# Performance work log

Hardware: AMD Instinct MI355X
Metric: run time of the kernel (lower is better)

The kernel has to match this reference:

```python
import jax, jax.numpy as jnp
import numpy as np

D_IN = 256
D_OUT = 256

def setup_inputs() -> dict:
    key = jax.random.key(0)
    kx, kq, kk, kv = jax.random.split(key, 4)
    x = jax.random.normal(kx, (8, D_IN, 64, 64), dtype=jnp.float32)
    s = 1.0 / np.sqrt(D_IN)
    Wq = jax.random.normal(kq, (D_OUT, D_IN), dtype=jnp.float32) * s
    Wk = jax.random.normal(kk, (D_OUT, D_IN), dtype=jnp.float32) * s
    Wv = jax.random.normal(kv, (D_OUT, D_IN), dtype=jnp.float32) * s
    return {"x": x, "Wq": Wq, "Wk": Wk, "Wv": Wv}

def reference(x, Wq, Wk, Wv):
    b, c_in, h, w = x.shape
    c = Wq.shape[0]
    # 1x1 conv == channel linear; tokens along N = h*w
    xt = x.reshape(b, c_in, h * w).transpose(0, 2, 1)      # (b, N, c_in)
    q = jnp.einsum('bnc,dc->bnd', xt, Wq)                  # (b, N, c)
    k = jnp.einsum('bnc,dc->bnd', xt, Wk)
    v = jnp.einsum('bnc,dc->bnd', xt, Wv)
    wei = jnp.einsum('bnd,bmd->bnm', q, k) / jnp.sqrt(jnp.asarray(c, x.dtype))
    wei = jax.nn.softmax(wei, axis=-1)
    out = jnp.einsum('bnm,bmd->bnd', wei, v)               # (b, N, c)
    return out.transpose(0, 2, 1).reshape(b, c, h, w)
```

## Files before the change

### kernel.cpp

```cpp
#include <hip/hip_runtime.h>

#define DIN 256
#define NTOK 4096

typedef __bf16 bf16;
typedef __bf16 bf16x4 __attribute__((ext_vector_type(4)));
typedef __bf16 bf16x8 __attribute__((ext_vector_type(8)));
typedef float floatx16 __attribute__((ext_vector_type(16)));

__device__ inline floatx16 mfma32(bf16x8 a, bf16x8 b, floatx16 c) {
    return __builtin_amdgcn_mfma_f32_32x32x16_bf16(a, b, c, 0, 0, 0);
}

__device__ inline void async16(const void* g, void* l) {
    __builtin_amdgcn_global_load_lds(
        (const __attribute__((address_space(1))) unsigned int*)g,
        (__attribute__((address_space(3))) unsigned int*)l, 16, 0, 0);
}

__global__ void convert_w(const float* __restrict__ wq, const float* __restrict__ wk,
                          const float* __restrict__ wv, bf16* __restrict__ Wb) {
    int i = blockIdx.x * 256 + threadIdx.x;
    const float* src = (i < 65536) ? wq : (i < 131072 ? wk : wv);
    Wb[i] = (bf16)src[i & 65535];
}

__global__ __launch_bounds__(512, 2) void proj_kernel(
    const float* __restrict__ x, const bf16* __restrict__ Wb,
    bf16* __restrict__ Qo, bf16* __restrict__ Ko, bf16* __restrict__ Vo)
{
    __shared__ __attribute__((aligned(16))) char smem[131072];
    bf16 (*xs)[264] = (bf16(*)[264])smem;
    bf16* bufA = (bf16*)smem;
    bf16* bufB = (bf16*)(smem + 65536);

    int bid = blockIdx.x;
    int b = bid & 7, nt = bid >> 3;
    int n0 = nt * 128;
    int t = threadIdx.x;
    int lane = t & 63, w = t >> 6;
    int l32 = lane & 31, h = lane >> 5;
    int tokg = w >> 1;
    int og   = w & 1;

    int wofs[8];
#pragma unroll
    for (int jj = 0; jj < 8; ++jj) {
        int q = w * 8 + jj;
        int r2 = 2 * q + h;
        int cs = l32 ^ (r2 & 31);
        wofs[jj] = r2 * 512 + cs * 16;
    }

    {
        const float* xb = x + (size_t)b * DIN * NTOK;
#pragma unroll
        for (int it = 0; it < 16; ++it) {
            int flat = it * 512 + t;
            int c = flat >> 5;
            int nf = flat & 31;
            float4 v = *(const float4*)(xb + (size_t)c * NTOK + n0 + nf * 4);
            int nn = nf * 4;
            xs[nn + 0][c] = (bf16)v.x;
            xs[nn + 1][c] = (bf16)v.y;
            xs[nn + 2][c] = (bf16)v.z;
            xs[nn + 3][c] = (bf16)v.w;
        }
    }
    __syncthreads();

    bf16x8 xf[16];
#pragma unroll
    for (int ks = 0; ks < 16; ++ks)
        xf[ks] = *(const bf16x8*)&xs[tokg * 32 + l32][ks * 16 + h * 8];

    __syncthreads();

    {
        const char* src = (const char*)Wb;
#pragma unroll
        for (int jj = 0; jj < 8; ++jj)
            async16(src + wofs[jj], (char*)bufA + (w * 8 + jj) * 1024);
    }
    __syncthreads();

    for (int p = 0; p < 6; ++p) {
        if (p < 5) {
            bf16* nb = ((p + 1) & 1) ? bufB : bufA;
            const char* src = (const char*)Wb + (size_t)(p + 1) * 65536;
#pragma unroll
            for (int jj = 0; jj < 8; ++jj)
                async16(src + wofs[jj], (char*)nb + (w * 8 + jj) * 1024);
        }

        const bf16* wb = (p & 1) ? bufB : bufA;
        int mat = p >> 1, dhalf = p & 1;

        floatx16 acc[2];
#pragma unroll
        for (int dc = 0; dc < 2; ++dc)
#pragma unroll
            for (int i = 0; i < 16; ++i) acc[dc][i] = 0.0f;

        if (mat < 2) {
#pragma unroll
            for (int ks = 0; ks < 16; ++ks) {
#pragma unroll
                for (int dc = 0; dc < 2; ++dc) {
                    int row = og * 64 + dc * 32 + l32;
                    bf16x8 wf = *(const bf16x8*)((const char*)wb + row * 512 +
                                                 (((2 * ks + h) ^ (row & 31)) * 16));
                    acc[dc] = mfma32(xf[ks], wf, acc[dc]);
                }
            }
            bf16* Out = (mat == 0 ? Qo : Ko) + (size_t)b * NTOK * DIN;
#pragma unroll
            for (int dc = 0; dc < 2; ++dc) {
                int d = dhalf * 128 + og * 64 + dc * 32 + l32;
#pragma unroll
                for (int r = 0; r < 16; ++r) {
                    int tok = n0 + tokg * 32 + (r & 3) + 8 * (r >> 2) + 4 * h;
                    Out[(size_t)tok * DIN + d] = (bf16)acc[dc][r];
                }
            }
        } else {
#pragma unroll
            for (int ks = 0; ks < 16; ++ks) {
#pragma unroll
                for (int dc = 0; dc < 2; ++dc) {
                    int row = og * 64 + dc * 32 + l32;
                    bf16x8 wf = *(const bf16x8*)((const char*)wb + row * 512 +
                                                 (((2 * ks + h) ^ (row & 31)) * 16));
                    acc[dc] = mfma32(wf, xf[ks], acc[dc]);
                }
            }
            bf16* Out = Vo + (size_t)b * DIN * NTOK;
            int tok = n0 + tokg * 32 + l32;
#pragma unroll
            for (int dc = 0; dc < 2; ++dc)
#pragma unroll
                for (int r = 0; r < 16; ++r) {
                    int d = dhalf * 128 + og * 64 + dc * 32 + (r & 3) + 8 * (r >> 2) + 4 * h;
                    Out[(size_t)d * NTOK + tok] = (bf16)acc[dc][r];
                }
        }
        __syncthreads();
    }
}

__global__ __launch_bounds__(768, 3) void attn_kernel(
    const bf16* __restrict__ Q, const bf16* __restrict__ K,
    const bf16* __restrict__ V, float* __restrict__ out)
{
    __shared__ bf16 Ks[2][64][256];
    __shared__ bf16 Vs[2][256][64];
    __shared__ bf16 Ps[2][128][64];

    int bid = blockIdx.x;
    int b = bid & 7, qt = bid >> 3;
    int n0 = qt * 128;
    int t = threadIdx.x, lane = t & 63, w = t >> 6;
    int l32 = lane & 31, h = lane >> 5;
    int lkey = (l32 & 7) ^ ((l32 >> 3) & 3);

    const bf16* Qb = Q + (size_t)b * NTOK * DIN;
    const bf16* Kb = K + (size_t)b * NTOK * DIN;
    const bf16* Vb = V + (size_t)b * DIN * NTOK;
    float* Lp = (float*)&Ps[0][0][0];

    if (w < 4) {
        int qg = w;

        int koff[8];
#pragma unroll
        for (int jj = 0; jj < 8; ++jj) {
            int q = w * 8 + jj;
            int r = q * 2 + h;
            int ck = l32 ^ ((r & 7) ^ ((r >> 3) & 3));
            koff[jj] = (r * 256 + ck * 8) * 2;
        }

        bf16x8 qf[16];
        {
            const bf16* qrow = Qb + (size_t)(n0 + qg * 32 + l32) * DIN + h * 8;
#pragma unroll
            for (int ks = 0; ks < 16; ++ks) qf[ks] = *(const bf16x8*)(qrow + ks * 16);
        }

        float lsum = 0.0f;

#pragma unroll
        for (int jj = 0; jj < 8; ++jj) {
            async16((const char*)Kb + koff[jj], (bf16*)Ks[0] + (w * 8 + jj) * 512);
            async16((const char*)Kb + 32768 + koff[jj], (bf16*)Ks[1] + (w * 8 + jj) * 512);
        }
        __syncthreads();

        {
            const bf16* Krd = (const bf16*)Ks[0] + l32 * 256;
            floatx16 st0, st1;
#pragma unroll
            for (int i = 0; i < 16; ++i) { st0[i] = 0.0f; st1[i] = 0.0f; }
#pragma unroll
            for (int ks = 0; ks < 16; ++ks) {
                int co = ((2 * ks + h) ^ lkey) * 8;
                bf16x8 kf0 = *(const bf16x8*)(Krd + co);
                bf16x8 kf1 = *(const bf16x8*)(Krd + 32 * 256 + co);
                st0 = mfma32(kf0, qf[ks], st0);
                st1 = mfma32(kf1, qf[ks], st1);
            }
            bf16* Prow = (bf16*)Ps[0] + (qg * 32 + l32) * 64;
#pragma unroll
            for (int kvb = 0; kvb < 2; ++kvb) {
#pragma unroll
                for (int g = 0; g < 4; ++g) {
                    bf16x4 pk;
#pragma unroll
                    for (int i = 0; i < 4; ++i) {
                        float sval = kvb ? st1[g * 4 + i] : st0[g * 4 + i];
                        float e = __expf(sval * 0.0625f);
                        lsum += e;
                        pk[i] = (bf16)e;
                    }
                    *(bf16x4*)((char*)Prow + (((kvb * 4 + g) ^ lkey) * 16) + h * 8) = pk;
                }
            }
        }
        __syncthreads();

#pragma unroll 1
        for (int mt = 0; mt < 64; ++mt) {
            if (mt < 62) {
                int kadd = (mt + 2) * 32768;
#pragma unroll
                for (int jj = 0; jj < 8; ++jj)
                    async16((const char*)Kb + kadd + koff[jj],
                            (bf16*)Ks[mt & 1] + (w * 8 + jj) * 512);
            }
            if (mt < 63) {
                const bf16* Krd = (const bf16*)Ks[(mt + 1) & 1] + l32 * 256;
                floatx16 st0, st1;
#pragma unroll
                for (int i = 0; i < 16; ++i) { st0[i] = 0.0f; st1[i] = 0.0f; }
#pragma unroll
                for (int ks = 0; ks < 16; ++ks) {
                    int co = ((2 * ks + h) ^ lkey) * 8;
                    bf16x8 kf0 = *(const bf16x8*)(Krd + co);
                    bf16x8 kf1 = *(const bf16x8*)(Krd + 32 * 256 + co);
                    st0 = mfma32(kf0, qf[ks], st0);
                    st1 = mfma32(kf1, qf[ks], st1);
                }
                bf16* Prow = (bf16*)Ps[(mt + 1) & 1] + (qg * 32 + l32) * 64;
#pragma unroll
                for (int kvb = 0; kvb < 2; ++kvb) {
#pragma unroll
                    for (int g = 0; g < 4; ++g) {
                        bf16x4 pk;
#pragma unroll
                        for (int i = 0; i < 4; ++i) {
                            float sval = kvb ? st1[g * 4 + i] : st0[g * 4 + i];
                            float e = __expf(sval * 0.0625f);
                            lsum += e;
                            pk[i] = (bf16)e;
                        }
                        *(bf16x4*)((char*)Prow + (((kvb * 4 + g) ^ lkey) * 16) + h * 8) = pk;
                    }
                }
            }
            __syncthreads();
        }

        {
            float sv = lsum;
            sv += __shfl_xor(sv, 32);
            if (h == 0) Lp[qg * 32 + l32] = sv;
        }
        __syncthreads();
    } else {
        int ws = w - 4;
        int slab2 = ws >> 1;
        int qh = ws & 1;

        int vofs[4];
#pragma unroll
        for (int jj = 0; jj < 4; ++jj) {
            int q = ws * 4 + jj;
            int d = q * 8 + (lane >> 3);
            int cv = (lane & 7) ^ ((d & 7) ^ ((d >> 3) & 3));
            vofs[jj] = (d * 4096 + cv * 8) * 2;
        }

        floatx16 oacc[4];
#pragma unroll
        for (int i = 0; i < 4; ++i)
            for (int j = 0; j < 16; ++j) oacc[i][j] = 0.0f;

#pragma unroll
        for (int jj = 0; jj < 4; ++jj)
            async16((const char*)Vb + vofs[jj], (bf16*)Vs[0] + (ws * 4 + jj) * 512);
        __syncthreads();
        __syncthreads();

#pragma unroll 1
        for (int mt = 0; mt < 64; ++mt) {
            if (mt < 63) {
                int vadd = (mt + 1) * 128;
#pragma unroll
                for (int jj = 0; jj < 4; ++jj)
                    async16((const char*)Vb + vadd + vofs[jj],
                            (bf16*)Vs[(mt + 1) & 1] + (ws * 4 + jj) * 512);
            }
            const bf16* Vrd = (const bf16*)Vs[mt & 1];
            const char* Prd = (const char*)Ps[mt & 1];
#pragma unroll
            for (int kst = 0; kst < 4; ++kst) {
                int co = ((kst * 2 + h) ^ lkey);
                int d0 = slab2 * 64 + l32;
                bf16x8 va0 = *(const bf16x8*)(Vrd + d0 * 64 + co * 8);
                bf16x8 va1 = *(const bf16x8*)(Vrd + (d0 + 32) * 64 + co * 8);
                bf16x8 pb0 = *(const bf16x8*)(Prd + (qh * 64 + l32) * 128 + co * 16);
                bf16x8 pb1 = *(const bf16x8*)(Prd + (qh * 64 + 32 + l32) * 128 + co * 16);
                oacc[0] = mfma32(va0, pb0, oacc[0]);
                oacc[1] = mfma32(va0, pb1, oacc[1]);
                oacc[2] = mfma32(va1, pb0, oacc[2]);
                oacc[3] = mfma32(va1, pb1, oacc[3]);
            }
            __syncthreads();
        }

        __syncthreads();
        float* ob = out + (size_t)b * DIN * NTOK;
#pragma unroll
        for (int tc = 0; tc < 2; ++tc) {
            int tokl = qh * 64 + tc * 32 + l32;
            float rinv = 1.0f / Lp[tokl];
#pragma unroll
            for (int dc = 0; dc < 2; ++dc)
#pragma unroll
                for (int r = 0; r < 16; ++r) {
                    int d = slab2 * 64 + dc * 32 + (r & 3) + 8 * (r >> 2) + 4 * h;
                    ob[(size_t)d * NTOK + n0 + tokl] = oacc[dc * 2 + tc][r] * rinv;
                }
        }
    }
}

extern "C" void kernel_launch(void* const* d_in, const int* in_sizes, int n_in,
                              void* d_out, int out_size, void* d_ws, size_t ws_size,
                              hipStream_t stream) {
    const float* x  = (const float*)d_in[0];
    const float* wq = (const float*)d_in[1];
    const float* wk = (const float*)d_in[2];
    const float* wv = (const float*)d_in[3];
    float* outf = (float*)d_out;

    char* ws = (char*)d_ws;
    bf16* Wb = (bf16*)(ws);
    bf16* Qp = (bf16*)(ws + (1u << 20));
    bf16* Kp = (bf16*)(ws + (1u << 20) + (16u << 20));
    bf16* Vp = (bf16*)(ws + (1u << 20) + (32u << 20));

    convert_w<<<768, 256, 0, stream>>>(wq, wk, wv, Wb);
    proj_kernel<<<256, 512, 0, stream>>>(x, Wb, Qp, Kp, Vp);
    attn_kernel<<<256, 768, 0, stream>>>(Qp, Kp, Vp, outf);
}
```

Measured before the change: 244.9 us.

## Fuse P·V into score waves via register-resident P and direct V loads

```diff
diff --git a/kernel.cpp b/kernel.cpp
--- a/kernel.cpp
+++ b/kernel.cpp
@@ -16,6 +16,20 @@
     __builtin_amdgcn_global_load_lds(
         (const __attribute__((address_space(1))) unsigned int*)g,
         (__attribute__((address_space(3))) unsigned int*)l, 16, 0, 0);
+}
+
+__device__ inline unsigned pkbf(float a, float b) {
+    union { bf16 e[2]; unsigned u; } x;
+    x.e[0] = (bf16)a; x.e[1] = (bf16)b;
+    return x.u;
+}
+
+__device__ inline bf16x8 mkfrag(int h, unsigned a0, unsigned a1, unsigned a2, unsigned a3,
+                                unsigned b0, unsigned b1, unsigned b2, unsigned b3) {
+    union { unsigned u[4]; bf16x8 v; } x;
+    x.u[0] = h ? b0 : a0; x.u[1] = h ? b1 : a1;
+    x.u[2] = h ? b2 : a2; x.u[3] = h ? b3 : a3;
+    return x.v;
 }
 
 __global__ void convert_w(const float* __restrict__ wq, const float* __restrict__ wk,
@@ -148,17 +162,70 @@
     }
 }
 
-__global__ __launch_bounds__(768, 3) void attn_kernel(
+
+#define TILE_COMPUTE(TILE, KS)                                                    \
+    {                                                                             \
+        const bf16* Krd = (const bf16*)(KS) + l32 * 256;                          \
+        floatx16 st0, st1;                                                        \
+        _Pragma("unroll")                                                         \
+        for (int i = 0; i < 16; ++i) { st0[i] = 0.0f; st1[i] = 0.0f; }            \
+        _Pragma("unroll")                                                         \
+        for (int ks = 0; ks < 16; ++ks) {                                         \
+            int co = ((2 * ks + h) ^ lkey) * 8;                                   \
+            bf16x8 kf0 = *(const bf16x8*)(Krd + co);                              \
+            bf16x8 kf1 = *(const bf16x8*)(Krd + 32 * 256 + co);                   \
+            st0 = mfma32(kf0, qf[ks], st0);                                       \
+            st1 = mfma32(kf1, qf[ks], st1);                                       \
+        }                                                                         \
+        _Pragma("unroll")                                                         \
+        for (int i = 0; i < 16; ++i) {                                            \
+            float e0 = __expf(st0[i] * 0.0625f); lsum += e0; st0[i] = e0;         \
+            float e1 = __expf(st1[i] * 0.0625f); lsum += e1; st1[i] = e1;         \
+        }                                                                         \
+        unsigned pA0 = pkbf(st0[0], st0[1]),   pB0 = pkbf(st0[2], st0[3]);        \
+        unsigned pC0 = pkbf(st0[4], st0[5]),   pD0 = pkbf(st0[6], st0[7]);        \
+        unsigned pE0 = pkbf(st0[8], st0[9]),   pF0 = pkbf(st0[10], st0[11]);      \
+        unsigned pG0 = pkbf(st0[12], st0[13]), pH0 = pkbf(st0[14], st0[15]);      \
+        unsigned pA1 = pkbf(st1[0], st1[1]),   pB1 = pkbf(st1[2], st1[3]);        \
+        unsigned pC1 = pkbf(st1[4], st1[5]),   pD1 = pkbf(st1[6], st1[7]);        \
+        unsigned pE1 = pkbf(st1[8], st1[9]),   pF1 = pkbf(st1[10], st1[11]);      \
+        unsigned pG1 = pkbf(st1[12], st1[13]), pH1 = pkbf(st1[14], st1[15]);      \
+        unsigned sA0 = __shfl_xor(pA0, 32), sB0 = __shfl_xor(pB0, 32);            \
+        unsigned sC0 = __shfl_xor(pC0, 32), sD0 = __shfl_xor(pD0, 32);            \
+        unsigned sE0 = __shfl_xor(pE0, 32), sF0 = __shfl_xor(pF0, 32);            \
+        unsigned sG0 = __shfl_xor(pG0, 32), sH0 = __shfl_xor(pH0, 32);            \
+        unsigned sA1 = __shfl_xor(pA1, 32), sB1 = __shfl_xor(pB1, 32);            \
+        unsigned sC1 = __shfl_xor(pC1, 32), sD1 = __shfl_xor(pD1, 32);            \
+        unsigned sE1 = __shfl_xor(pE1, 32), sF1 = __shfl_xor(pF1, 32);            \
+        unsigned sG1 = __shfl_xor(pG1, 32), sH1 = __shfl_xor(pH1, 32);            \
+        bf16x8 pb0 = mkfrag(h, pA0, pB0, sA0, sB0, sC0, sD0, pC0, pD0);           \
+        bf16x8 pb1 = mkfrag(h, pE0, pF0, sE0, sF0, sG0, sH0, pG0, pH0);           \
+        bf16x8 pb2 = mkfrag(h, pA1, pB1, sA1, sB1, sC1, sD1, pC1, pD1);           \
+        bf16x8 pb3 = mkfrag(h, pE1, pF1, sE1, sF1, sG1, sH1, pG1, pH1);           \
+        const bf16* Vt = Vb + (TILE) * 64 + h * 8;                                \
+        _Pragma("unroll")                                                         \
+        for (int db = 0; db < 8; ++db) {                                          \
+            const bf16* vrow = Vt + (size_t)(db * 32 + l32) * NTOK;               \
+            bf16x8 va0 = *(const bf16x8*)(vrow);                                  \
+            bf16x8 va1 = *(const bf16x8*)(vrow + 16);                             \
+            bf16x8 va2 = *(const bf16x8*)(vrow + 32);                             \
+            bf16x8 va3 = *(const bf16x8*)(vrow + 48);                             \
+            oacc[db] = mfma32(va0, pb0, oacc[db]);                                \
+            oacc[db] = mfma32(va1, pb1, oacc[db]);                                \
+            oacc[db] = mfma32(va2, pb2, oacc[db]);                                \
+            oacc[db] = mfma32(va3, pb3, oacc[db]);                                \
+        }                                                                         \
+    }
+
+__global__ __launch_bounds__(128, 1) void attn_kernel(
     const bf16* __restrict__ Q, const bf16* __restrict__ K,
     const bf16* __restrict__ V, float* __restrict__ out)
 {
     __shared__ bf16 Ks[2][64][256];
-    __shared__ bf16 Vs[2][256][64];
-    __shared__ bf16 Ps[2][128][64];
 
     int bid = blockIdx.x;
     int b = bid & 7, qt = bid >> 3;
-    int n0 = qt * 128;
+    int n0 = qt * 64;
     int t = threadIdx.x, lane = t & 63, w = t >> 6;
     int l32 = lane & 31, h = lane >> 5;
     int lkey = (l32 & 7) ^ ((l32 >> 3) & 3);
@@ -166,183 +233,64 @@
     const bf16* Qb = Q + (size_t)b * NTOK * DIN;
     const bf16* Kb = K + (size_t)b * NTOK * DIN;
     const bf16* Vb = V + (size_t)b * DIN * NTOK;
-    float* Lp = (float*)&Ps[0][0][0];
-
-    if (w < 4) {
-        int qg = w;
-
-        int koff[8];
-#pragma unroll
-        for (int jj = 0; jj < 8; ++jj) {
-            int q = w * 8 + jj;
-            int r = q * 2 + h;
-            int ck = l32 ^ ((r & 7) ^ ((r >> 3) & 3));
-            koff[jj] = (r * 256 + ck * 8) * 2;
-        }
-
-        bf16x8 qf[16];
-        {
-            const bf16* qrow = Qb + (size_t)(n0 + qg * 32 + l32) * DIN + h * 8;
-#pragma unroll
-            for (int ks = 0; ks < 16; ++ks) qf[ks] = *(const bf16x8*)(qrow + ks * 16);
-        }
-
-        float lsum = 0.0f;
-
-#pragma unroll
-        for (int jj = 0; jj < 8; ++jj) {
-            async16((const char*)Kb + koff[jj], (bf16*)Ks[0] + (w * 8 + jj) * 512);
-            async16((const char*)Kb + 32768 + koff[jj], (bf16*)Ks[1] + (w * 8 + jj) * 512);
-        }
+
+    int koff[16];
+#pragma unroll
+    for (int jj = 0; jj < 16; ++jj) {
+        int q = w * 16 + jj;
+        int r = 2 * q + h;
+        int ck = l32 ^ ((r & 7) ^ ((r >> 3) & 3));
+        koff[jj] = (r * 256 + ck * 8) * 2;
+    }
+
+    bf16x8 qf[16];
+    {
+        const bf16* qrow = Qb + (size_t)(n0 + w * 32 + l32) * DIN + h * 8;
+#pragma unroll
+        for (int ks = 0; ks < 16; ++ks) qf[ks] = *(const bf16x8*)(qrow + ks * 16);
+    }
+
+    floatx16 oacc[8];
+#pragma unroll
+    for (int i = 0; i < 8; ++i)
+#pragma unroll
+        for (int j = 0; j < 16; ++j) oacc[i][j] = 0.0f;
+    float lsum = 0.0f;
+
+#pragma unroll
+    for (int jj = 0; jj < 16; ++jj) {
+        async16((const char*)Kb + koff[jj], (bf16*)Ks[0] + (w * 16 + jj) * 512);
+        async16((const char*)Kb + 32768 + koff[jj], (bf16*)Ks[1] + (w * 16 + jj) * 512);
+    }
+    __syncthreads();
+
+    TILE_COMPUTE(0, Ks[0]);
+    __syncthreads();
+
+#pragma unroll 1
+    for (int mt = 0; mt < 63; ++mt) {
+        if (mt < 62) {
+            int kadd = (mt + 2) * 32768;
+#pragma unroll
+            for (int jj = 0; jj < 16; ++jj)
+                async16((const char*)Kb + kadd + koff[jj],
+                        (bf16*)Ks[mt & 1] + (w * 16 + jj) * 512);
+        }
+        TILE_COMPUTE(mt + 1, Ks[(mt + 1) & 1]);
         __syncthreads();
-
-        {
-            const bf16* Krd = (const bf16*)Ks[0] + l32 * 256;
-            floatx16 st0, st1;
-#pragma unroll
-            for (int i = 0; i < 16; ++i) { st0[i] = 0.0f; st1[i] = 0.0f; }
-#pragma unroll
-            for (int ks = 0; ks < 16; ++ks) {
-                int co = ((2 * ks + h) ^ lkey) * 8;
-                bf16x8 kf0 = *(const bf16x8*)(Krd + co);
-                bf16x8 kf1 = *(const bf16x8*)(Krd + 32 * 256 + co);
-                st0 = mfma32(kf0, qf[ks], st0);
-                st1 = mfma32(kf1, qf[ks], st1);
-            }
-            bf16* Prow = (bf16*)Ps[0] + (qg * 32 + l32) * 64;
-#pragma unroll
-            for (int kvb = 0; kvb < 2; ++kvb) {
-#pragma unroll
-                for (int g = 0; g < 4; ++g) {
-                    bf16x4 pk;
-#pragma unroll
-                    for (int i = 0; i < 4; ++i) {
-                        float sval = kvb ? st1[g * 4 + i] : st0[g * 4 + i];
-                        float e = __expf(sval * 0.0625f);
-                        lsum += e;
-                        pk[i] = (bf16)e;
-                    }
-                    *(bf16x4*)((char*)Prow + (((kvb * 4 + g) ^ lkey) * 16) + h * 8) = pk;
-                }
-            }
-        }
-        __syncthreads();
-
-#pragma unroll 1
-        for (int mt = 0; mt < 64; ++mt) {
-            if (mt < 62) {
-                int kadd = (mt + 2) * 32768;
-#pragma unroll
-                for (int jj = 0; jj < 8; ++jj)
-                    async16((const char*)Kb + kadd + koff[jj],
-                            (bf16*)Ks[mt & 1] + (w * 8 + jj) * 512);
-            }
-            if (mt < 63) {
-                const bf16* Krd = (const bf16*)Ks[(mt + 1) & 1] + l32 * 256;
-                floatx16 st0, st1;
-#pragma unroll
-                for (int i = 0; i < 16; ++i) { st0[i] = 0.0f; st1[i] = 0.0f; }
-#pragma unroll
-                for (int ks = 0; ks < 16; ++ks) {
-                    int co = ((2 * ks + h) ^ lkey) * 8;
-                    bf16x8 kf0 = *(const bf16x8*)(Krd + co);
-                    bf16x8 kf1 = *(const bf16x8*)(Krd + 32 * 256 + co);
-                    st0 = mfma32(kf0, qf[ks], st0);
-                    st1 = mfma32(kf1, qf[ks], st1);
-                }
-                bf16* Prow = (bf16*)Ps[(mt + 1) & 1] + (qg * 32 + l32) * 64;
-#pragma unroll
-                for (int kvb = 0; kvb < 2; ++kvb) {
-#pragma unroll
-                    for (int g = 0; g < 4; ++g) {
-                        bf16x4 pk;
-#pragma unroll
-                        for (int i = 0; i < 4; ++i) {
-                            float sval = kvb ? st1[g * 4 + i] : st0[g * 4 + i];
-                            float e = __expf(sval * 0.0625f);
-                            lsum += e;
-                            pk[i] = (bf16)e;
-                        }
-                        *(bf16x4*)((char*)Prow + (((kvb * 4 + g) ^ lkey) * 16) + h * 8) = pk;
-                    }
-                }
-            }
-            __syncthreads();
-        }
-
-        {
-            float sv = lsum;
-            sv += __shfl_xor(sv, 32);
-            if (h == 0) Lp[qg * 32 + l32] = sv;
-        }
-        __syncthreads();
-    } else {
-        int ws = w - 4;
-        int slab2 = ws >> 1;
-        int qh = ws & 1;
-
-        int vofs[4];
-#pragma unroll
-        for (int jj = 0; jj < 4; ++jj) {
-            int q = ws * 4 + jj;
-            int d = q * 8 + (lane >> 3);
-            int cv = (lane & 7) ^ ((d & 7) ^ ((d >> 3) & 3));
-            vofs[jj] = (d * 4096 + cv * 8) * 2;
-        }
-
-        floatx16 oacc[4];
-#pragma unroll
-        for (int i = 0; i < 4; ++i)
-            for (int j = 0; j < 16; ++j) oacc[i][j] = 0.0f;
-
-#pragma unroll
-        for (int jj = 0; jj < 4; ++jj)
-            async16((const char*)Vb + vofs[jj], (bf16*)Vs[0] + (ws * 4 + jj) * 512);
-        __syncthreads();
-        __syncthreads();
-
-#pragma unroll 1
-        for (int mt = 0; mt < 64; ++mt) {
-            if (mt < 63) {
-                int vadd = (mt + 1) * 128;
-#pragma unroll
-                for (int jj = 0; jj < 4; ++jj)
-                    async16((const char*)Vb + vadd + vofs[jj],
-                            (bf16*)Vs[(mt + 1) & 1] + (ws * 4 + jj) * 512);
-            }
-            const bf16* Vrd = (const bf16*)Vs[mt & 1];
-            const char* Prd = (const char*)Ps[mt & 1];
-#pragma unroll
-            for (int kst = 0; kst < 4; ++kst) {
-                int co = ((kst * 2 + h) ^ lkey);
-                int d0 = slab2 * 64 + l32;
-                bf16x8 va0 = *(const bf16x8*)(Vrd + d0 * 64 + co * 8);
-                bf16x8 va1 = *(const bf16x8*)(Vrd + (d0 + 32) * 64 + co * 8);
-                bf16x8 pb0 = *(const bf16x8*)(Prd + (qh * 64 + l32) * 128 + co * 16);
-                bf16x8 pb1 = *(const bf16x8*)(Prd + (qh * 64 + 32 + l32) * 128 + co * 16);
-                oacc[0] = mfma32(va0, pb0, oacc[0]);
-                oacc[1] = mfma32(va0, pb1, oacc[1]);
-                oacc[2] = mfma32(va1, pb0, oacc[2]);
-                oacc[3] = mfma32(va1, pb1, oacc[3]);
-            }
-            __syncthreads();
-        }
-
-        __syncthreads();
-        float* ob = out + (size_t)b * DIN * NTOK;
-#pragma unroll
-        for (int tc = 0; tc < 2; ++tc) {
-            int tokl = qh * 64 + tc * 32 + l32;
-            float rinv = 1.0f / Lp[tokl];
-#pragma unroll
-            for (int dc = 0; dc < 2; ++dc)
-#pragma unroll
-                for (int r = 0; r < 16; ++r) {
-                    int d = slab2 * 64 + dc * 32 + (r & 3) + 8 * (r >> 2) + 4 * h;
-                    ob[(size_t)d * NTOK + n0 + tokl] = oacc[dc * 2 + tc][r] * rinv;
-                }
-        }
-    }
+    }
+
+    float tot = lsum + __shfl_xor(lsum, 32);
+    float rinv = 1.0f / tot;
+    float* ob = out + (size_t)b * DIN * NTOK;
+    int tok = n0 + w * 32 + l32;
+#pragma unroll
+    for (int db = 0; db < 8; ++db)
+#pragma unroll
+        for (int r = 0; r < 16; ++r) {
+            int d = db * 32 + (r & 3) + 8 * (r >> 2) + 4 * h;
+            ob[(size_t)d * NTOK + tok] = oacc[db][r] * rinv;
+        }
 }
 
 extern "C" void kernel_launch(void* const* d_in, const int* in_sizes, int n_in,
@@ -362,5 +310,5 @@
 
     convert_w<<<768, 256, 0, stream>>>(wq, wk, wv, Wb);
     proj_kernel<<<256, 512, 0, stream>>>(x, Wb, Qp, Kp, Vp);
-    attn_kernel<<<256, 768, 0, stream>>>(Qp, Kp, Vp, outf);
-}
+    attn_kernel<<<512, 128, 0, stream>>>(Qp, Kp, Vp, outf);
+}
```

After: 366.6 us. +49.6%, slower.
